# Kernel tuning notes

Measured on AMD Instinct MI355X. Metric: run time of the kernel, lower is better.

## Reference

```python
import jax, jax.numpy as jnp
import numpy as np

N_EMBD = 1024
N_HEAD = 16
DIM_HEAD = N_EMBD // N_HEAD
SCALE = DIM_HEAD ** (-0.5)  # source divides by this (i.e. multiplies scores by sqrt(dim_head))


def setup_inputs() -> dict:
    key = jax.random.key(0)
    k1, k2, k3, k4, k5 = jax.random.split(key, 5)
    B, Tq, Tkv = 2, 2048, 2048
    x_q = jax.random.normal(k1, (B, Tq, N_EMBD), dtype=jnp.float32)
    x_kv = jax.random.normal(k2, (B, Tkv, N_EMBD), dtype=jnp.float32)
    s = 0.02
    W_q = jax.random.normal(k3, (N_EMBD, N_EMBD), dtype=jnp.float32) * s
    W_kv = jax.random.normal(k4, (N_EMBD, 2 * N_EMBD), dtype=jnp.float32) * s
    W_proj = jax.random.normal(k5, (N_EMBD, N_EMBD), dtype=jnp.float32) * s
    return {"x_q": x_q, "x_kv": x_kv, "W_q": W_q, "W_kv": W_kv, "W_proj": W_proj}


def reference(x_q, x_kv, W_q, W_kv, W_proj):
    B, Tq, C = x_q.shape
    Tkv = x_kv.shape[1]
    q = x_q @ W_q                      # [B, Tq, C]
    kv = x_kv @ W_kv                   # [B, Tkv, 2C]
    k, v = jnp.split(kv, 2, axis=2)
    # [B, H, T, Dh]
    q = q.reshape(B, Tq, N_HEAD, DIM_HEAD).transpose(0, 2, 1, 3)
    k = k.reshape(B, Tkv, N_HEAD, DIM_HEAD).transpose(0, 2, 1, 3)
    v = v.reshape(B, Tkv, N_HEAD, DIM_HEAD).transpose(0, 2, 1, 3)
    # Faithful to source: scores = q@k^T / scale  (== * sqrt(dim_head))
    attn = jnp.einsum('bhqd,bhkd->bhqk', q, k) / SCALE
    attn = jax.nn.softmax(attn, axis=-1)
    y = jnp.einsum('bhqk,bhkd->bhqd', attn, v)
    y = y.transpose(0, 2, 1, 3).reshape(B, Tq, C)
    return y @ W_proj
```

## Files before the change

### kernel.cpp

```cpp
#include <hip/hip_runtime.h>
#include <cstddef>

typedef _Float16 f16;
typedef _Float16 f16x8 __attribute__((ext_vector_type(8)));
typedef _Float16 f16x4 __attribute__((ext_vector_type(4)));
typedef _Float16 f16x2 __attribute__((ext_vector_type(2)));
typedef float f32x4 __attribute__((ext_vector_type(4)));
typedef float f32x16 __attribute__((ext_vector_type(16)));
typedef unsigned int u32;

__device__ inline float exp2_fast(float x) {
  float r;
  asm("v_exp_f32 %0, %1" : "=v"(r) : "v"(x));
  return r;
}

__global__ __launch_bounds__(256) void prep(
    const float* __restrict__ xq, const float* __restrict__ xkv,
    f16* __restrict__ oq, f16* __restrict__ okv,
    const float* __restrict__ Wq, const float* __restrict__ Wkv,
    const float* __restrict__ Wp, f16* __restrict__ Wqt,
    f16* __restrict__ Wkvt, f16* __restrict__ Wpt) {
  __shared__ float t[32][33];
  int bid = blockIdx.x;
  if (bid < 8192) {
    const float* in = (bid < 4096) ? xq : xkv;
    f16* out = (bid < 4096) ? oq : okv;
    int i = ((bid & 4095) * 256 + threadIdx.x) * 4;
    float4 v = *(const float4*)&in[i];
    f16x4 h;
    h[0] = (f16)v.x; h[1] = (f16)v.y; h[2] = (f16)v.z; h[3] = (f16)v.w;
    *(f16x4*)&out[i] = h;
  } else {
    int zz = bid - 8192;
    int bx = zz & 31, by = (zz >> 5) & 31, z = zz >> 10;
    const float* in;
    f16* out;
    int N = 1024, extra = 0;
    if (z == 0) { in = Wq; out = Wqt; }
    else if (z == 3) { in = Wp; out = Wpt; }
    else { in = Wkv; out = Wkvt; N = 2048; extra = (z - 1) * 1024; }
    int tx = threadIdx.x % 32, ty = threadIdx.x / 32;
    int n0 = bx * 32 + extra, k0 = by * 32;
#pragma unroll
    for (int i = 0; i < 32; i += 8)
      t[ty + i][tx] = in[(size_t)(k0 + ty + i) * N + n0 + tx];
    __syncthreads();
#pragma unroll
    for (int i = 0; i < 32; i += 8)
      out[(size_t)(n0 + ty + i) * 1024 + k0 + tx] = (f16)t[tx][ty + i];
  }
}

template <int BN, typename CT>
__device__ __forceinline__ void gemm_body(
    const f16* __restrict__ A, const f16* __restrict__ Bt, CT* __restrict__ C,
    int bid, int M, int N, int K, float scale, f16* As, f16* Bs) {
  constexpr int NT = BN / 32;
  constexpr int BI = BN / 32;
  const int nb = N / BN;
  const int m0 = (bid / nb) * 128;
  const int n0 = (bid % nb) * BN;
  const int tid = threadIdx.x;
  const int w = tid >> 6, lane = tid & 63;
  const int l16 = lane & 15, quad = lane >> 4;
  const int wrow = (w >> 1) * 64, wcol = (w & 1) * (BN / 2);
  const int sr = tid >> 3, sc8 = tid & 7;
  const int wc8 = sc8 ^ (sr & 7);

  f32x4 acc[4][NT] = {};
  f16x8 ar[4], br[BI];

#pragma unroll
  for (int i = 0; i < 4; i++)
    ar[i] = *(const f16x8*)&A[(size_t)(m0 + sr + i * 32) * K + sc8 * 8];
#pragma unroll
  for (int i = 0; i < BI; i++)
    br[i] = *(const f16x8*)&Bt[(size_t)(n0 + sr + i * 32) * K + sc8 * 8];

  for (int k0 = 0; k0 < K; k0 += 64) {
#pragma unroll
    for (int i = 0; i < 4; i++)
      *(f16x8*)&As[(sr + i * 32) * 64 + wc8 * 8] = ar[i];
#pragma unroll
    for (int i = 0; i < BI; i++)
      *(f16x8*)&Bs[(sr + i * 32) * 64 + wc8 * 8] = br[i];
    __syncthreads();

    if (k0 + 64 < K) {
#pragma unroll
      for (int i = 0; i < 4; i++)
        ar[i] = *(const f16x8*)&A[(size_t)(m0 + sr + i * 32) * K + k0 + 64 + sc8 * 8];
#pragma unroll
      for (int i = 0; i < BI; i++)
        br[i] = *(const f16x8*)&Bt[(size_t)(n0 + sr + i * 32) * K + k0 + 64 + sc8 * 8];
    }

    f16x8 bf[NT][2];
#pragma unroll
    for (int nt = 0; nt < NT; nt++) {
      const int row = wcol + nt * 16 + l16;
#pragma unroll
      for (int s = 0; s < 2; s++)
        bf[nt][s] = *(const f16x8*)&Bs[row * 64 + (((s * 4 + quad) ^ (row & 7)) << 3)];
    }
#pragma unroll
    for (int mt = 0; mt < 4; mt++) {
      const int row = wrow + mt * 16 + l16;
      f16x8 af0 = *(const f16x8*)&As[row * 64 + ((quad ^ (row & 7)) << 3)];
      f16x8 af1 = *(const f16x8*)&As[row * 64 + (((4 + quad) ^ (row & 7)) << 3)];
#pragma unroll
      for (int nt = 0; nt < NT; nt++) {
        acc[mt][nt] = __builtin_amdgcn_mfma_f32_16x16x32_f16(af0, bf[nt][0], acc[mt][nt], 0, 0, 0);
        acc[mt][nt] = __builtin_amdgcn_mfma_f32_16x16x32_f16(af1, bf[nt][1], acc[mt][nt], 0, 0, 0);
      }
    }
    __syncthreads();
  }

#pragma unroll
  for (int mt = 0; mt < 4; mt++)
#pragma unroll
    for (int nt = 0; nt < NT; nt++)
#pragma unroll
      for (int r = 0; r < 4; r++) {
        int row = m0 + wrow + mt * 16 + quad * 4 + r;
        int col = n0 + wcol + nt * 16 + l16;
        C[(size_t)row * N + col] = (CT)(acc[mt][nt][r] * scale);
      }
}

__global__ __launch_bounds__(256, 3) void qkv_gemm(
    const f16* __restrict__ Xq, const f16* __restrict__ Wqt, f16* __restrict__ Qh,
    const f16* __restrict__ Xkv, const f16* __restrict__ Wkvt, f16* __restrict__ KVh,
    float sc_q) {
  __shared__ f16 As[128 * 64];
  __shared__ f16 Bs[128 * 64];
  if (blockIdx.x < 256)
    gemm_body<128, f16>(Xq, Wqt, Qh, blockIdx.x, 4096, 1024, 1024, sc_q, As, Bs);
  else
    gemm_body<128, f16>(Xkv, Wkvt, KVh, blockIdx.x - 256, 4096, 2048, 1024, 1.0f, As, Bs);
}

template <int BN, typename CT>
__global__ __launch_bounds__(256, 2) void gemm_lds(
    const f16* __restrict__ A, const f16* __restrict__ Bt, CT* __restrict__ C,
    int M, int N, int K, float scale) {
  __shared__ f16 As[128 * 64];
  __shared__ f16 Bs[BN * 64];
  gemm_body<BN, CT>(A, Bt, C, blockIdx.x, M, N, K, scale, As, Bs);
}

__global__ __launch_bounds__(256) void attn_kernel(
    const f16* __restrict__ Qh, const f16* __restrict__ KVh, f16* __restrict__ Yh) {
  __shared__ f16 smem[18432];
  f16* Ks = smem;
  f16* Vt = smem + 64 * 72;
  f16* Ps = smem + 2 * 64 * 72;

  const int bid = blockIdx.x;
  const int hb = bid & 31;
  const int qt = bid >> 5;
  const int h = hb >> 1, b = hb & 1;
  const int tid = threadIdx.x;
  const int w = tid >> 6, lane = tid & 63;
  const int l31 = lane & 31, e = lane >> 5;

  const size_t qrow0 = (size_t)b * 2048 + (size_t)qt * 128;
  const size_t kvrow0 = (size_t)b * 2048;
  f16* Psw = Ps + w * 32 * 72;

  f16x8 qf[4];
#pragma unroll
  for (int ks = 0; ks < 4; ks++)
    qf[ks] = *(const f16x8*)&Qh[(qrow0 + w * 32 + l31) * 1024 + h * 64 + ks * 16 + e * 8];

  float m_run = -1e30f, l_run = 0.0f;
  f32x16 o_acc[2] = {};

  const int ksr = tid >> 2, ksc = (tid & 3) << 4;
  const int vkv0 = (tid >> 3) * 2;
  const int vd0 = (tid & 7) * 8;
  const int vcol = ((((vkv0 >> 3) ^ (tid & 7)) << 3) | (vkv0 & 7));

  f16x8 kr0, kr1, vr0, vr1;
  {
    const f16* kb = &KVh[(kvrow0 + ksr) * 2048 + h * 64 + ksc];
    kr0 = *(const f16x8*)kb;
    kr1 = *(const f16x8*)(kb + 8);
    const f16* vb = &KVh[(kvrow0 + vkv0) * 2048 + 1024 + h * 64 + vd0];
    vr0 = *(const f16x8*)vb;
    vr1 = *(const f16x8*)(vb + 2048);
  }

  for (int t = 0; t < 32; t++) {
    *(f16x8*)&Ks[ksr * 72 + ksc] = kr0;
    *(f16x8*)&Ks[ksr * 72 + ksc + 8] = kr1;
#pragma unroll
    for (int j = 0; j < 8; j++) {
      f16x2 p; p[0] = vr0[j]; p[1] = vr1[j];
      *(f16x2*)&Vt[(vd0 + j) * 72 + vcol] = p;
    }
    __syncthreads();

    if (t + 1 < 32) {
      const f16* kb = &KVh[(kvrow0 + (t + 1) * 64 + ksr) * 2048 + h * 64 + ksc];
      kr0 = *(const f16x8*)kb;
      kr1 = *(const f16x8*)(kb + 8);
      const f16* vb = &KVh[(kvrow0 + (t + 1) * 64 + vkv0) * 2048 + 1024 + h * 64 + vd0];
      vr0 = *(const f16x8*)vb;
      vr1 = *(const f16x8*)(vb + 2048);
    }

    f32x16 sacc[2] = {};
#pragma unroll
    for (int kvt = 0; kvt < 2; kvt++)
#pragma unroll
      for (int ks = 0; ks < 4; ks++) {
        f16x8 a = *(const f16x8*)&Ks[(kvt * 32 + l31) * 72 + ks * 16 + e * 8];
        sacc[kvt] = __builtin_amdgcn_mfma_f32_32x32x16_f16(a, qf[ks], sacc[kvt], 0, 0, 0);
      }

    float mx = sacc[0][0];
#pragma unroll
    for (int r = 1; r < 16; r++) mx = fmaxf(mx, sacc[0][r]);
#pragma unroll
    for (int r = 0; r < 16; r++) mx = fmaxf(mx, sacc[1][r]);
    mx = fmaxf(mx, __shfl_xor(mx, 32, 64));
    float mnew = fmaxf(m_run, mx);
    float alpha = exp2_fast(m_run - mnew);
    m_run = mnew;

    float ssum = 0.0f;
#pragma unroll
    for (int kvt = 0; kvt < 2; kvt++)
#pragma unroll
      for (int r = 0; r < 16; r++) {
        float p = exp2_fast(sacc[kvt][r] - mnew);
        sacc[kvt][r] = p;
        ssum += p;
      }
    ssum += __shfl_xor(ssum, 32, 64);
    l_run = l_run * alpha + ssum;
#pragma unroll
    for (int r = 0; r < 16; r++) { o_acc[0][r] *= alpha; o_acc[1][r] *= alpha; }

#pragma unroll
    for (int kvt = 0; kvt < 2; kvt++)
#pragma unroll
      for (int r2 = 0; r2 < 4; r2++) {
        f16x4 hh;
        hh[0] = (f16)sacc[kvt][r2 * 4 + 0];
        hh[1] = (f16)sacc[kvt][r2 * 4 + 1];
        hh[2] = (f16)sacc[kvt][r2 * 4 + 2];
        hh[3] = (f16)sacc[kvt][r2 * 4 + 3];
        *(f16x4*)&Psw[l31 * 72 + kvt * 32 + r2 * 8 + e * 4] = hh;
      }

    f16x8 pf[4];
#pragma unroll
    for (int ks = 0; ks < 4; ks++)
      pf[ks] = *(const f16x8*)&Psw[l31 * 72 + ks * 16 + e * 8];
#pragma unroll
    for (int dt = 0; dt < 2; dt++) {
      const int d = dt * 32 + l31;
      const int dx = d >> 3;
#pragma unroll
      for (int ks = 0; ks < 4; ks++) {
        f16x8 va = *(const f16x8*)&Vt[d * 72 + (((ks * 2 + e) ^ dx) << 3)];
        o_acc[dt] = __builtin_amdgcn_mfma_f32_32x32x16_f16(va, pf[ks], o_acc[dt], 0, 0, 0);
      }
    }
    __syncthreads();
  }

  float linv = 1.0f / l_run;
  float* Of = (float*)smem + w * 2176;
#pragma unroll
  for (int dt = 0; dt < 2; dt++)
#pragma unroll
    for (int r2 = 0; r2 < 4; r2++) {
      f32x4 vv;
      vv[0] = o_acc[dt][r2 * 4 + 0] * linv;
      vv[1] = o_acc[dt][r2 * 4 + 1] * linv;
      vv[2] = o_acc[dt][r2 * 4 + 2] * linv;
      vv[3] = o_acc[dt][r2 * 4 + 3] * linv;
      *(f32x4*)&Of[l31 * 68 + dt * 32 + r2 * 8 + e * 4] = vv;
    }
  const int qq = lane >> 1, dh = (lane & 1) * 32;
#pragma unroll
  for (int j = 0; j < 8; j++) {
    f32x4 v = *(const f32x4*)&Of[qq * 68 + dh + j * 4];
    f16x4 hh;
    hh[0] = (f16)v[0]; hh[1] = (f16)v[1]; hh[2] = (f16)v[2]; hh[3] = (f16)v[3];
    *(f16x4*)&Yh[(qrow0 + w * 32 + qq) * 1024 + h * 64 + dh + j * 4] = hh;
  }
}

extern "C" void kernel_launch(void* const* d_in, const int* in_sizes, int n_in,
                              void* d_out, int out_size, void* d_ws, size_t ws_size,
                              hipStream_t stream) {
  const float* x_q  = (const float*)d_in[0];
  const float* x_kv = (const float*)d_in[1];
  const float* W_q  = (const float*)d_in[2];
  const float* W_kv = (const float*)d_in[3];
  const float* W_p  = (const float*)d_in[4];
  float* out = (float*)d_out;

  f16* Wq_t  = (f16*)d_ws;
  f16* Wkv_t = Wq_t  + (size_t)1024 * 1024;
  f16* Wp_t  = Wkv_t + (size_t)2048 * 1024;
  f16* Qh    = Wp_t  + (size_t)1024 * 1024;
  f16* KVh   = Qh    + (size_t)4096 * 1024;
  f16* Yh    = KVh   + (size_t)4096 * 2048;
  f16* Xq_h  = Yh;
  f16* Xkv_h = Yh    + (size_t)4096 * 1024;

  prep<<<12288, 256, 0, stream>>>(x_q, x_kv, Xq_h, Xkv_h,
                                  W_q, W_kv, W_p, Wq_t, Wkv_t, Wp_t);

  const float SC = 11.5415603f;
  qkv_gemm<<<768, 256, 0, stream>>>(Xq_h, Wq_t, Qh, Xkv_h, Wkv_t, KVh, SC);

  attn_kernel<<<512, 256, 0, stream>>>(Qh, KVh, Yh);

  gemm_lds<64, float><<<512, 256, 0, stream>>>(Yh, Wp_t, out, 4096, 1024, 1024, 1.0f);
}
```

Baseline: 205.6 us.

## Keep softmax probabilities in registers via permlane32 swap and skip lazy rescales

The P tile is no longer sent through LDS. Probabilities are packed to f16 in registers with cvt_pkrtz and reshuffled into MFMA B-operand layout with v_permlane32_swap, which removes the per-tile LDS store and load and halves shared memory. The online softmax now rescales the running max and the accumulators only when the new max exceeds the old one by more than 8 in the log2 domain. This is a wave-uniform conditional skip that stays exact after final normalisation, though unnormalised values may grow. The max and sum reductions use tree/multi-accumulator forms, and the epilogue writes f16 through LDS with wider stores.

Result: no change. 207.1 us (+0.7%).

```diff
diff --git a/kernel.cpp b/kernel.cpp
--- a/kernel.cpp
+++ b/kernel.cpp
@@ -13,6 +13,18 @@
   float r;
   asm("v_exp_f32 %0, %1" : "=v"(r) : "v"(x));
   return r;
+}
+
+__device__ inline int pk2(float x, float y) {
+  return __builtin_bit_cast(int, __builtin_amdgcn_cvt_pkrtz(x, y));
+}
+
+__device__ inline f16x2 pk2h(float x, float y) {
+  return __builtin_bit_cast(f16x2, __builtin_amdgcn_cvt_pkrtz(x, y));
+}
+
+__device__ inline void permlane32_swap(int& a, int& b) {
+  asm volatile("v_permlane32_swap_b32 %0, %1" : "+v"(a), "+v"(b));
 }
 
 __global__ __launch_bounds__(256) void prep(
@@ -153,10 +165,9 @@
 
 __global__ __launch_bounds__(256) void attn_kernel(
     const f16* __restrict__ Qh, const f16* __restrict__ KVh, f16* __restrict__ Yh) {
-  __shared__ f16 smem[18432];
+  __shared__ f16 smem[9216];
   f16* Ks = smem;
   f16* Vt = smem + 64 * 72;
-  f16* Ps = smem + 2 * 64 * 72;
 
   const int bid = blockIdx.x;
   const int hb = bid & 31;
@@ -168,7 +179,6 @@
 
   const size_t qrow0 = (size_t)b * 2048 + (size_t)qt * 128;
   const size_t kvrow0 = (size_t)b * 2048;
-  f16* Psw = Ps + w * 32 * 72;
 
   f16x8 qf[4];
 #pragma unroll
@@ -221,46 +231,61 @@
         sacc[kvt] = __builtin_amdgcn_mfma_f32_32x32x16_f16(a, qf[ks], sacc[kvt], 0, 0, 0);
       }
 
-    float mx = sacc[0][0];
-#pragma unroll
-    for (int r = 1; r < 16; r++) mx = fmaxf(mx, sacc[0][r]);
-#pragma unroll
-    for (int r = 0; r < 16; r++) mx = fmaxf(mx, sacc[1][r]);
+    float mxa[4];
+#pragma unroll
+    for (int j = 0; j < 4; j++) {
+      float a = fmaxf(fmaxf(sacc[0][j], sacc[0][j + 4]),
+                      fmaxf(sacc[0][j + 8], sacc[0][j + 12]));
+      float bb = fmaxf(fmaxf(sacc[1][j], sacc[1][j + 4]),
+                       fmaxf(sacc[1][j + 8], sacc[1][j + 12]));
+      mxa[j] = fmaxf(a, bb);
+    }
+    float mx = fmaxf(fmaxf(mxa[0], mxa[1]), fmaxf(mxa[2], mxa[3]));
     mx = fmaxf(mx, __shfl_xor(mx, 32, 64));
-    float mnew = fmaxf(m_run, mx);
-    float alpha = exp2_fast(m_run - mnew);
-    m_run = mnew;
-
-    float ssum = 0.0f;
+
+    if (!__all(mx <= m_run + 8.0f)) {
+      float mnew = fmaxf(m_run, mx);
+      float alpha = exp2_fast(m_run - mnew);
+      m_run = mnew;
+      l_run *= alpha;
+#pragma unroll
+      for (int r = 0; r < 16; r++) { o_acc[0][r] *= alpha; o_acc[1][r] *= alpha; }
+    }
+
+    float ss0 = 0.0f, ss1 = 0.0f, ss2 = 0.0f, ss3 = 0.0f;
 #pragma unroll
     for (int kvt = 0; kvt < 2; kvt++)
 #pragma unroll
-      for (int r = 0; r < 16; r++) {
-        float p = exp2_fast(sacc[kvt][r] - mnew);
-        sacc[kvt][r] = p;
-        ssum += p;
-      }
+      for (int r = 0; r < 16; r += 4) {
+        float p0 = exp2_fast(sacc[kvt][r + 0] - m_run);
+        float p1 = exp2_fast(sacc[kvt][r + 1] - m_run);
+        float p2 = exp2_fast(sacc[kvt][r + 2] - m_run);
+        float p3 = exp2_fast(sacc[kvt][r + 3] - m_run);
+        sacc[kvt][r + 0] = p0; sacc[kvt][r + 1] = p1;
+        sacc[kvt][r + 2] = p2; sacc[kvt][r + 3] = p3;
+        ss0 += p0; ss1 += p1; ss2 += p2; ss3 += p3;
+      }
+    float ssum = (ss0 + ss1) + (ss2 + ss3);
     ssum += __shfl_xor(ssum, 32, 64);
-    l_run = l_run * alpha + ssum;
-#pragma unroll
-    for (int r = 0; r < 16; r++) { o_acc[0][r] *= alpha; o_acc[1][r] *= alpha; }
-
+    l_run += ssum;
+
+    f16x8 pf[4];
 #pragma unroll
     for (int kvt = 0; kvt < 2; kvt++)
 #pragma unroll
-      for (int r2 = 0; r2 < 4; r2++) {
-        f16x4 hh;
-        hh[0] = (f16)sacc[kvt][r2 * 4 + 0];
-        hh[1] = (f16)sacc[kvt][r2 * 4 + 1];
-        hh[2] = (f16)sacc[kvt][r2 * 4 + 2];
-        hh[3] = (f16)sacc[kvt][r2 * 4 + 3];
-        *(f16x4*)&Psw[l31 * 72 + kvt * 32 + r2 * 8 + e * 4] = hh;
-      }
-
-    f16x8 pf[4];
-#pragma unroll
-    for (int ks = 0; ks < 4; ks++)
-      pf[ks] = *(const f16x8*)&Psw[l31 * 72 + ks * 16 + e * 8];
+      for (int half = 0; half < 2; half++) {
+        const int h8 = half * 8;
+        int a0 = pk2(sacc[kvt][h8 + 0], sacc[kvt][h8 + 1]);
+        int b0 = pk2(sacc[kvt][h8 + 4], sacc[kvt][h8 + 5]);
+        int a1 = pk2(sacc[kvt][h8 + 2], sacc[kvt][h8 + 3]);
+        int b1 = pk2(sacc[kvt][h8 + 6], sacc[kvt][h8 + 7]);
+        permlane32_swap(a0, b0);
+        permlane32_swap(a1, b1);
+        union { int i[4]; f16x8 v; } u;
+        u.i[0] = a0; u.i[1] = a1; u.i[2] = b0; u.i[3] = b1;
+        pf[kvt * 2 + half] = u.v;
+      }
+
 #pragma unroll
     for (int dt = 0; dt < 2; dt++) {
       const int d = dt * 32 + l31;
@@ -275,25 +300,21 @@
   }
 
   float linv = 1.0f / l_run;
-  float* Of = (float*)smem + w * 2176;
+  f16* Of = smem + w * 32 * 72;
 #pragma unroll
   for (int dt = 0; dt < 2; dt++)
 #pragma unroll
     for (int r2 = 0; r2 < 4; r2++) {
-      f32x4 vv;
-      vv[0] = o_acc[dt][r2 * 4 + 0] * linv;
-      vv[1] = o_acc[dt][r2 * 4 + 1] * linv;
-      vv[2] = o_acc[dt][r2 * 4 + 2] * linv;
-      vv[3] = o_acc[dt][r2 * 4 + 3] * linv;
-      *(f32x4*)&Of[l31 * 68 + dt * 32 + r2 * 8 + e * 4] = vv;
+      f16x2 h0 = pk2h(o_acc[dt][r2 * 4 + 0] * linv, o_acc[dt][r2 * 4 + 1] * linv);
+      f16x2 h1 = pk2h(o_acc[dt][r2 * 4 + 2] * linv, o_acc[dt][r2 * 4 + 3] * linv);
+      f16x4 hh; hh[0] = h0[0]; hh[1] = h0[1]; hh[2] = h1[0]; hh[3] = h1[1];
+      *(f16x4*)&Of[l31 * 72 + dt * 32 + r2 * 8 + e * 4] = hh;
     }
   const int qq = lane >> 1, dh = (lane & 1) * 32;
 #pragma unroll
-  for (int j = 0; j < 8; j++) {
-    f32x4 v = *(const f32x4*)&Of[qq * 68 + dh + j * 4];
-    f16x4 hh;
-    hh[0] = (f16)v[0]; hh[1] = (f16)v[1]; hh[2] = (f16)v[2]; hh[3] = (f16)v[3];
-    *(f16x4*)&Yh[(qrow0 + w * 32 + qq) * 1024 + h * 64 + dh + j * 4] = hh;
+  for (int j = 0; j < 4; j++) {
+    f16x8 v = *(const f16x8*)&Of[qq * 72 + dh + j * 8];
+    *(f16x8*)&Yh[(qrow0 + w * 32 + qq) * 1024 + h * 64 + dh + j * 8] = v;
   }
 }
 
```
